# Performance work log

Measured on AMD Instinct MI355X. Metric: run time of the kernel, lower is better.

Reference implementation:

```python
import jax, jax.numpy as jnp
import numpy as np

N_BITS = 8
QMAX = 2 ** (N_BITS - 1) - 1  # 127 for int8 symmetric
EPS = 1e-8


def fake_quant(x, axis):
    """Symmetric per-slice (row/col) dynamic fake quantization with STE-compatible form."""
    amax = jnp.max(jnp.abs(x), axis=axis, keepdims=True)
    scale = jnp.maximum(amax, EPS) / QMAX
    q = jnp.clip(jnp.round(x / scale), -QMAX - 1, QMAX) * scale
    return q


def setup_inputs() -> dict:
    key = jax.random.key(0)
    k1, k2 = jax.random.split(key)
    inputs1 = jax.random.normal(k1, (2, 16, 2048, 128), dtype=jnp.float32)
    inputs2 = jax.random.normal(k2, (2, 16, 128, 2048), dtype=jnp.float32)
    return {"inputs1": inputs1, "inputs2": inputs2}


def reference(inputs1, inputs2):
    # input1: row-wise (axes=-1) quant; input2: axes=-1 (module default); output: row-wise
    q1 = fake_quant(inputs1, axis=-1)
    q2 = fake_quant(inputs2, axis=-1)
    out = jnp.matmul(q1, q2)  # [B, H, S, S]
    return fake_quant(out, axis=-1)
```

## Files before the change

### kernel.cpp

```cpp
#include <hip/hip_runtime.h>
#include <hip/hip_bf16.h>
#include <cstdint>

#define QMAXF 127.0f
#define EPSQ 1e-8f

typedef __bf16 bf16x8 __attribute__((ext_vector_type(8)));
typedef float f32x4 __attribute__((ext_vector_type(4)));

static constexpr int BB = 32;
static constexpr int MM = 2048;
static constexpr int KK = 128;
static constexpr int NN = 2048;

static constexpr size_t OFF_Q1   = 0;
static constexpr size_t OFF_Q2T  = OFF_Q1  + (size_t)BB*MM*KK*2;
static constexpr size_t OFF_S1   = OFF_Q2T + (size_t)BB*NN*KK*2;
static constexpr size_t OFF_S2   = OFF_S1  + (size_t)BB*MM*4;

__global__ __launch_bounds__(256) void quant_rows128(const float* __restrict__ x,
                                                     unsigned short* __restrict__ q,
                                                     float* __restrict__ s1) {
    int wave = threadIdx.x >> 6, lane = threadIdx.x & 63;
    int row = blockIdx.x * 4 + wave;
    const float2* xr = reinterpret_cast<const float2*>(x) + (size_t)row * 64;
    float2 v = xr[lane];
    float a = fmaxf(fabsf(v.x), fabsf(v.y));
#pragma unroll
    for (int m = 32; m; m >>= 1) a = fmaxf(a, __shfl_xor(a, m));
    float scale = fmaxf(a, EPSQ) / QMAXF;
    float i0 = fminf(fmaxf(rintf(v.x / scale), -128.f), 127.f);
    float i1 = fminf(fmaxf(rintf(v.y / scale), -128.f), 127.f);
    __bf16 h0 = (__bf16)i0, h1 = (__bf16)i1;
    ushort2 st;
    st.x = *reinterpret_cast<unsigned short*>(&h0);
    st.y = *reinterpret_cast<unsigned short*>(&h1);
    reinterpret_cast<ushort2*>(q + (size_t)row * 128)[lane ^ ((row & 7) << 2)] = st;
    if (lane == 0) s1[row] = scale;
}

__global__ __launch_bounds__(256) void amax_rows2048(const float* __restrict__ x,
                                                     float* __restrict__ s2) {
    int row = blockIdx.x;
    const float4* xr = reinterpret_cast<const float4*>(x) + (size_t)row * 512;
    int t = threadIdx.x;
    float4 v0 = xr[t], v1 = xr[t + 256];
    float a = fmaxf(fmaxf(fmaxf(fabsf(v0.x), fabsf(v0.y)), fmaxf(fabsf(v0.z), fabsf(v0.w))),
                    fmaxf(fmaxf(fabsf(v1.x), fabsf(v1.y)), fmaxf(fabsf(v1.z), fabsf(v1.w))));
#pragma unroll
    for (int m = 32; m; m >>= 1) a = fmaxf(a, __shfl_xor(a, m));
    __shared__ float red[4];
    if ((t & 63) == 0) red[t >> 6] = a;
    __syncthreads();
    if (t == 0) {
        float m0 = fmaxf(fmaxf(red[0], red[1]), fmaxf(red[2], red[3]));
        s2[row] = fmaxf(m0, EPSQ) / QMAXF;
    }
}

__global__ __launch_bounds__(256) void quant_transpose(const float* __restrict__ x,
                                                       const float* __restrict__ s2,
                                                       unsigned short* __restrict__ q2t) {
    int b = blockIdx.x >> 5;
    int n0 = (blockIdx.x & 31) * 64;
    __shared__ unsigned short lds[64][136];
    int t = threadIdx.x;
    int rr = t >> 4, cc = t & 15;
#pragma unroll
    for (int p = 0; p < 8; ++p) {
        int k = p * 16 + rr;
        float s = s2[b * 128 + k];
        const float4* src = reinterpret_cast<const float4*>(x + ((size_t)b * 128 + k) * 2048 + n0);
        float4 v = src[cc];
        float f[4] = {v.x, v.y, v.z, v.w};
#pragma unroll
        for (int e = 0; e < 4; ++e) {
            float iq = fminf(fmaxf(rintf(f[e] / s), -128.f), 127.f);
            __bf16 h = (__bf16)(iq * s);
            lds[cc * 4 + e][k] = *reinterpret_cast<unsigned short*>(&h);
        }
    }
    __syncthreads();
    int nl = t >> 2, seg = t & 3;
    int sw = nl & 7;
    uint4* dstrow = reinterpret_cast<uint4*>(q2t + ((size_t)b * 2048 + n0 + nl) * 128);
#pragma unroll
    for (int j = 0; j < 4; ++j)
        dstrow[(seg * 4 + j) ^ sw] = *reinterpret_cast<const uint4*>(&lds[nl][seg * 32 + j * 8]);
}

__global__ __launch_bounds__(256, 2) void gemm_fused(const unsigned short* __restrict__ qa,
                                                     const unsigned short* __restrict__ qbt,
                                                     const float* __restrict__ s1,
                                                     float* __restrict__ out) {
    int id = blockIdx.x;
    int nid = (id & 7) * 64 + (id >> 3);
    int b = nid >> 4, mt = nid & 15;

    __shared__ unsigned short Bt[2][16384];
    __shared__ float rowAmax[128], sOsc[128], sQs[128], sS1[128];

    int tid = threadIdx.x, wave = tid >> 6, lane = tid & 63;
    if (tid < 128) {
        rowAmax[tid] = 0.f;
        sS1[tid] = s1[b * 2048 + mt * 128 + tid];
    }

    {
        const char* Ag = (const char*)(qa + (size_t)(b * 16 + mt) * 16384);
        const char* Bg = (const char*)(qbt + (size_t)(b * 16) * 16384);
        char* lA = (char*)&Bt[1][0];
        char* lB = (char*)&Bt[0][0];
#pragma unroll
        for (int i = 0; i < 8; ++i) {
            int off = i * 4096 + wave * 1024;
            __builtin_amdgcn_global_load_lds(
                (const __attribute__((address_space(1))) uint32_t*)(Ag + off + lane * 16),
                (__attribute__((address_space(3))) uint32_t*)(lA + off), 16, 0, 0);
            __builtin_amdgcn_global_load_lds(
                (const __attribute__((address_space(1))) uint32_t*)(Bg + off + lane * 16),
                (__attribute__((address_space(3))) uint32_t*)(lB + off), 16, 0, 0);
        }
    }
    __syncthreads();

    int wm = wave >> 1, wn = wave & 1;
    int lr = lane & 15, lg = lane >> 4;
    int swz = (lr & 7) << 3;

    bf16x8 afr[4][4];
#pragma unroll
    for (int ks = 0; ks < 4; ++ks)
#pragma unroll
        for (int mi = 0; mi < 4; ++mi)
            afr[ks][mi] = *reinterpret_cast<const bf16x8*>(
                &Bt[1][(wm * 64 + mi * 16 + lr) * 128 + ((ks * 32 + lg * 8) ^ swz)]);
    __syncthreads();

    size_t ob = (size_t)b * 2048 * 2048;
    float rmax[4] = {0.f, 0.f, 0.f, 0.f};

    for (int it = 0; it < 32; ++it) {
        int cur = it & 1;
        if (it < 31) {
            int nnt = (it + 1) & 15;
            const char* Bg = (const char*)(qbt + (size_t)(b * 16 + nnt) * 16384);
            char* lB = (char*)&Bt[cur ^ 1][0];
#pragma unroll
            for (int i = 0; i < 8; ++i) {
                int off = i * 4096 + wave * 1024;
                __builtin_amdgcn_global_load_lds(
                    (const __attribute__((address_space(1))) uint32_t*)(Bg + off + lane * 16),
                    (__attribute__((address_space(3))) uint32_t*)(lB + off), 16, 0, 0);
            }
        }
        __builtin_amdgcn_sched_barrier(0);

        if (it == 16) {
            if (tid < 128) {
                float am = rowAmax[tid] * sS1[tid];
                float osc = fmaxf(am, EPSQ) / QMAXF;
                sOsc[tid] = osc;
                sQs[tid] = sS1[tid] / osc;
            }
            __syncthreads();
        }

        f32x4 acc[4][4];
#pragma unroll
        for (int mi = 0; mi < 4; ++mi)
#pragma unroll
            for (int ni = 0; ni < 4; ++ni) {
                f32x4 z = {0.f, 0.f, 0.f, 0.f};
                acc[mi][ni] = z;
            }

#pragma unroll
        for (int ks = 0; ks < 4; ++ks) {
            int kb = (ks * 32 + lg * 8) ^ swz;
            bf16x8 bfr[4];
#pragma unroll
            for (int ni = 0; ni < 4; ++ni)
                bfr[ni] = *reinterpret_cast<const bf16x8*>(&Bt[cur][(wn * 64 + ni * 16 + lr) * 128 + kb]);
#pragma unroll
            for (int mi = 0; mi < 4; ++mi)
#pragma unroll
                for (int ni = 0; ni < 4; ++ni)
                    acc[mi][ni] = __builtin_amdgcn_mfma_f32_16x16x32_bf16(bfr[ni], afr[ks][mi], acc[mi][ni], 0, 0, 0);
        }

        if (it < 16) {
#pragma unroll
            for (int mi = 0; mi < 4; ++mi)
#pragma unroll
                for (int ni = 0; ni < 4; ++ni)
#pragma unroll
                    for (int r = 0; r < 4; ++r)
                        rmax[mi] = fmaxf(rmax[mi], fabsf(acc[mi][ni][r]));
            if (it == 15) {
#pragma unroll
                for (int mi = 0; mi < 4; ++mi) {
                    float v = rmax[mi];
                    v = fmaxf(v, __shfl_xor(v, 16));
                    v = fmaxf(v, __shfl_xor(v, 32));
                    if (lg == 0) {
                        int row = wm * 64 + mi * 16 + lr;
                        atomicMax(reinterpret_cast<unsigned*>(&rowAmax[row]), __float_as_uint(v));
                    }
                }
            }
            __syncthreads();
        } else {
            int nt = it & 15;
#pragma unroll
            for (int mi = 0; mi < 4; ++mi) {
                int row = wm * 64 + mi * 16 + lr;
                float qs = sQs[row], osc = sOsc[row];
                size_t rowoff = ob + (size_t)(mt * 128 + row) * 2048 + nt * 128 + wn * 64 + lg * 4;
#pragma unroll
                for (int ni = 0; ni < 4; ++ni) {
                    f32x4 qv;
                    qv[0] = fminf(fmaxf(rintf(acc[mi][ni][0] * qs), -128.f), 127.f) * osc;
                    qv[1] = fminf(fmaxf(rintf(acc[mi][ni][1] * qs), -128.f), 127.f) * osc;
                    qv[2] = fminf(fmaxf(rintf(acc[mi][ni][2] * qs), -128.f), 127.f) * osc;
                    qv[3] = fminf(fmaxf(rintf(acc[mi][ni][3] * qs), -128.f), 127.f) * osc;
                    *reinterpret_cast<f32x4*>(&out[rowoff + ni * 16]) = qv;
                }
            }
            asm volatile("s_waitcnt vmcnt(16) lgkmcnt(0)" ::: "memory");
            __builtin_amdgcn_s_barrier();
        }
    }
}

extern "C" void kernel_launch(void* const* d_in, const int* in_sizes, int n_in,
                              void* d_out, int out_size, void* d_ws, size_t ws_size,
                              hipStream_t stream) {
    const float* in1 = (const float*)d_in[0];
    const float* in2 = (const float*)d_in[1];
    char* ws = (char*)d_ws;
    unsigned short* q1  = (unsigned short*)(ws + OFF_Q1);
    unsigned short* q2t = (unsigned short*)(ws + OFF_Q2T);
    float* s1   = (float*)(ws + OFF_S1);
    float* s2   = (float*)(ws + OFF_S2);
    float* out  = (float*)d_out;

    quant_rows128 <<<BB * MM / 4, 256, 0, stream>>>(in1, q1, s1);
    amax_rows2048 <<<BB * KK,     256, 0, stream>>>(in2, s2);
    quant_transpose<<<BB * (NN / 64), 256, 0, stream>>>(in2, s2, q2t);
    gemm_fused    <<<BB * 16,     256, 0, stream>>>(q1, q2t, s1, out);
}
```

Before: 215.3 us.

## Split two-pass loop and read B directly from global in output pass

Restructures the fused 32-iteration loop into a first pass that computes row amax via LDS-staged B tiles, then a second pass that recomputes the matmul reading B fragments straight from global memory. This removes the LDS prefetch and the per-iteration barriers and waitcnt from the store-heavy quantize pass. In exchange, it loses prefetch overlap and depends on cache hits for the global B loads.

Result: slower. 220.8 us (+2.5%).

```diff
diff --git a/kernel.cpp b/kernel.cpp
--- a/kernel.cpp
+++ b/kernel.cpp
@@ -140,11 +140,10 @@
     size_t ob = (size_t)b * 2048 * 2048;
     float rmax[4] = {0.f, 0.f, 0.f, 0.f};
 
-    for (int it = 0; it < 32; ++it) {
+    for (int it = 0; it < 16; ++it) {
         int cur = it & 1;
-        if (it < 31) {
-            int nnt = (it + 1) & 15;
-            const char* Bg = (const char*)(qbt + (size_t)(b * 16 + nnt) * 16384);
+        if (it < 15) {
+            const char* Bg = (const char*)(qbt + (size_t)(b * 16 + it + 1) * 16384);
             char* lB = (char*)&Bt[cur ^ 1][0];
 #pragma unroll
             for (int i = 0; i < 8; ++i) {
@@ -154,17 +153,6 @@
                     (__attribute__((address_space(3))) uint32_t*)(lB + off), 16, 0, 0);
             }
         }
-        __builtin_amdgcn_sched_barrier(0);
-
-        if (it == 16) {
-            if (tid < 128) {
-                float am = rowAmax[tid] * sS1[tid];
-                float osc = fmaxf(am, EPSQ) / QMAXF;
-                sOsc[tid] = osc;
-                sQs[tid] = sS1[tid] / osc;
-            }
-            __syncthreads();
-        }
 
         f32x4 acc[4][4];
 #pragma unroll
@@ -174,7 +162,6 @@
                 f32x4 z = {0.f, 0.f, 0.f, 0.f};
                 acc[mi][ni] = z;
             }
-
 #pragma unroll
         for (int ks = 0; ks < 4; ++ks) {
             int kb = (ks * 32 + lg * 8) ^ swz;
@@ -188,47 +175,73 @@
                 for (int ni = 0; ni < 4; ++ni)
                     acc[mi][ni] = __builtin_amdgcn_mfma_f32_16x16x32_bf16(bfr[ni], afr[ks][mi], acc[mi][ni], 0, 0, 0);
         }
-
-        if (it < 16) {
+#pragma unroll
+        for (int mi = 0; mi < 4; ++mi)
+#pragma unroll
+            for (int ni = 0; ni < 4; ++ni)
+#pragma unroll
+                for (int r = 0; r < 4; ++r)
+                    rmax[mi] = fmaxf(rmax[mi], fabsf(acc[mi][ni][r]));
+        __syncthreads();
+    }
+
+#pragma unroll
+    for (int mi = 0; mi < 4; ++mi) {
+        float v = rmax[mi];
+        v = fmaxf(v, __shfl_xor(v, 16));
+        v = fmaxf(v, __shfl_xor(v, 32));
+        if (lg == 0) {
+            int row = wm * 64 + mi * 16 + lr;
+            atomicMax(reinterpret_cast<unsigned*>(&rowAmax[row]), __float_as_uint(v));
+        }
+    }
+    __syncthreads();
+    if (tid < 128) {
+        float am = rowAmax[tid] * sS1[tid];
+        float osc = fmaxf(am, EPSQ) / QMAXF;
+        sOsc[tid] = osc;
+        sQs[tid] = sS1[tid] / osc;
+    }
+    __syncthreads();
+
+    const unsigned short* Bimg = qbt + (size_t)b * 16 * 16384;
+    for (int nt = 0; nt < 16; ++nt) {
+        f32x4 acc[4][4];
+#pragma unroll
+        for (int mi = 0; mi < 4; ++mi)
+#pragma unroll
+            for (int ni = 0; ni < 4; ++ni) {
+                f32x4 z = {0.f, 0.f, 0.f, 0.f};
+                acc[mi][ni] = z;
+            }
+#pragma unroll
+        for (int ks = 0; ks < 4; ++ks) {
+            int kb = (ks * 32 + lg * 8) ^ swz;
+            bf16x8 bfr[4];
+#pragma unroll
+            for (int ni = 0; ni < 4; ++ni)
+                bfr[ni] = *reinterpret_cast<const bf16x8*>(
+                    &Bimg[(size_t)(nt * 128 + wn * 64 + ni * 16 + lr) * 128 + kb]);
 #pragma unroll
             for (int mi = 0; mi < 4; ++mi)
 #pragma unroll
                 for (int ni = 0; ni < 4; ++ni)
-#pragma unroll
-                    for (int r = 0; r < 4; ++r)
-                        rmax[mi] = fmaxf(rmax[mi], fabsf(acc[mi][ni][r]));
-            if (it == 15) {
-#pragma unroll
-                for (int mi = 0; mi < 4; ++mi) {
-                    float v = rmax[mi];
-                    v = fmaxf(v, __shfl_xor(v, 16));
-                    v = fmaxf(v, __shfl_xor(v, 32));
-                    if (lg == 0) {
-                        int row = wm * 64 + mi * 16 + lr;
-                        atomicMax(reinterpret_cast<unsigned*>(&rowAmax[row]), __float_as_uint(v));
-                    }
-                }
-            }
-            __syncthreads();
-        } else {
-            int nt = it & 15;
-#pragma unroll
-            for (int mi = 0; mi < 4; ++mi) {
-                int row = wm * 64 + mi * 16 + lr;
-                float qs = sQs[row], osc = sOsc[row];
-                size_t rowoff = ob + (size_t)(mt * 128 + row) * 2048 + nt * 128 + wn * 64 + lg * 4;
-#pragma unroll
-                for (int ni = 0; ni < 4; ++ni) {
-                    f32x4 qv;
-                    qv[0] = fminf(fmaxf(rintf(acc[mi][ni][0] * qs), -128.f), 127.f) * osc;
-                    qv[1] = fminf(fmaxf(rintf(acc[mi][ni][1] * qs), -128.f), 127.f) * osc;
-                    qv[2] = fminf(fmaxf(rintf(acc[mi][ni][2] * qs), -128.f), 127.f) * osc;
-                    qv[3] = fminf(fmaxf(rintf(acc[mi][ni][3] * qs), -128.f), 127.f) * osc;
-                    *reinterpret_cast<f32x4*>(&out[rowoff + ni * 16]) = qv;
-                }
-            }
-            asm volatile("s_waitcnt vmcnt(16) lgkmcnt(0)" ::: "memory");
-            __builtin_amdgcn_s_barrier();
+                    acc[mi][ni] = __builtin_amdgcn_mfma_f32_16x16x32_bf16(bfr[ni], afr[ks][mi], acc[mi][ni], 0, 0, 0);
+        }
+#pragma unroll
+        for (int mi = 0; mi < 4; ++mi) {
+            int row = wm * 64 + mi * 16 + lr;
+            float qs = sQs[row], osc = sOsc[row];
+            size_t rowoff = ob + (size_t)(mt * 128 + row) * 2048 + nt * 128 + wn * 64 + lg * 4;
+#pragma unroll
+            for (int ni = 0; ni < 4; ++ni) {
+                f32x4 qv;
+                qv[0] = fminf(fmaxf(rintf(acc[mi][ni][0] * qs), -128.f), 127.f) * osc;
+                qv[1] = fminf(fmaxf(rintf(acc[mi][ni][1] * qs), -128.f), 127.f) * osc;
+                qv[2] = fminf(fmaxf(rintf(acc[mi][ni][2] * qs), -128.f), 127.f) * osc;
+                qv[3] = fminf(fmaxf(rintf(acc[mi][ni][3] * qs), -128.f), 127.f) * osc;
+                *reinterpret_cast<f32x4*>(&out[rowoff + ni * 16]) = qv;
+            }
         }
     }
 }
```
